# Kernel tuning notes

Hardware: AMD Instinct MI355X
Metric: run time of the kernel (lower is better)

Reference implementation:

```python
import jax, jax.numpy as jnp
import numpy as np

SCALE = 1.0

def setup_inputs() -> dict:
    key = jax.random.key(0)
    k1, k2 = jax.random.split(key)
    template = jax.random.normal(k1, (4, 8192, 3), dtype=jnp.float32)
    source = jax.random.normal(k2, (4, 8192, 3), dtype=jnp.float32)
    return {"template": template, "source": source}

def _chamfer(p0, p1):
    # p0: [B,N,3], p1: [B,M,3]
    # squared pairwise distances: [B,N,M]
    sq0 = jnp.sum(p0 * p0, axis=-1)  # [B,N]
    sq1 = jnp.sum(p1 * p1, axis=-1)  # [B,M]
    cross = jnp.einsum('bnd,bmd->bnm', p0, p1)
    d = sq0[:, :, None] + sq1[:, None, :] - 2.0 * cross  # [B,N,M]
    d = jnp.maximum(d, 0.0)
    cost_p0_p1 = jnp.min(d, axis=2)  # [B,N] min sq dist p0 -> p1
    cost_p1_p0 = jnp.min(d, axis=1)  # [B,M] min sq dist p1 -> p0
    c01 = jnp.mean(jnp.sqrt(cost_p0_p1), axis=-1)  # [B]
    c10 = jnp.mean(jnp.sqrt(cost_p1_p0), axis=-1)  # [B]
    return (c01 + c10) / 2.0  # [B]

def reference(template, source):
    p0 = template / SCALE
    p1 = source / SCALE
    per_batch = _chamfer(p0, p1)
    return jnp.mean(per_batch, axis=0)  # reduction='mean' -> scalar
```

## Files before the change

kernel.cpp:

```cpp
#include <hip/hip_runtime.h>
#include <math.h>

#define NPTS 8192
#define NB 4
#define BLK 256
#define Q 8
#define TILE 512

__global__ __launch_bounds__(BLK) void chamfer_partial(
    const float* __restrict__ tmpl, const float* __restrict__ src,
    float* __restrict__ partial, int seg_len, int nseg)
{
    __shared__ float4 lds[TILE];
    const int bd  = blockIdx.z;
    const int b   = bd >> 1;
    const int dir = bd & 1;
    const float* qp = (dir ? src : tmpl) + (size_t)b * NPTS * 3;
    const float* rp = (dir ? tmpl : src) + (size_t)b * NPTS * 3;
    const int tid   = threadIdx.x;
    const int qbase = blockIdx.x * (BLK * Q);

    float qx[Q], qy[Q], qz[Q], mn[Q];
#pragma unroll
    for (int k = 0; k < Q; k++) {
        const int qi = qbase + k * BLK + tid;
        qx[k] = qp[3 * qi + 0];
        qy[k] = qp[3 * qi + 1];
        qz[k] = qp[3 * qi + 2];
        mn[k] = 3.4e38f;
    }

    const int seg_start = blockIdx.y * seg_len;
    for (int ts = 0; ts < seg_len; ts += TILE) {
        __syncthreads();
        for (int i = tid; i < TILE; i += BLK) {
            const int ri = seg_start + ts + i;
            const float rx = rp[3 * ri + 0];
            const float ry = rp[3 * ri + 1];
            const float rz = rp[3 * ri + 2];
            lds[i] = make_float4(-2.f * rx, -2.f * ry, -2.f * rz,
                                 rx * rx + ry * ry + rz * rz);
        }
        __syncthreads();
#pragma unroll 4
        for (int j = 0; j < TILE; j++) {
            const float4 r = lds[j];
#pragma unroll
            for (int k = 0; k < Q; k++) {
                float t = fmaf(qx[k], r.x, r.w);
                t = fmaf(qy[k], r.y, t);
                t = fmaf(qz[k], r.z, t);
                mn[k] = fminf(mn[k], t);
            }
        }
    }

    const size_t base = ((size_t)bd * nseg + blockIdx.y) * NPTS;
#pragma unroll
    for (int k = 0; k < Q; k++)
        partial[base + qbase + k * BLK + tid] = mn[k];
}

__global__ __launch_bounds__(BLK) void chamfer_reduce(
    const float* __restrict__ tmpl, const float* __restrict__ src,
    const float* __restrict__ partial, float* __restrict__ out, int nseg)
{
    const int t  = blockIdx.x * BLK + threadIdx.x;
    const int bd = t >> 13;
    const int qi = t & (NPTS - 1);
    const int b  = bd >> 1;
    const int dir = bd & 1;
    const float* qp = (dir ? src : tmpl) + (size_t)b * NPTS * 3;
    const float qx = qp[3 * qi + 0];
    const float qy = qp[3 * qi + 1];
    const float qz = qp[3 * qi + 2];
    const float sq = qx * qx + qy * qy + qz * qz;

    float m = 3.4e38f;
    for (int s = 0; s < nseg; s++)
        m = fminf(m, partial[((size_t)bd * nseg + s) * NPTS + qi]);

    float v = sqrtf(fmaxf(sq + m, 0.f));

#pragma unroll
    for (int off = 32; off > 0; off >>= 1)
        v += __shfl_down(v, off, 64);

    __shared__ float wsum[BLK / 64];
    const int lane = threadIdx.x & 63;
    const int wid  = threadIdx.x >> 6;
    if (lane == 0) wsum[wid] = v;
    __syncthreads();
    if (threadIdx.x == 0) {
        float s = 0.f;
#pragma unroll
        for (int w = 0; w < BLK / 64; w++) s += wsum[w];
        atomicAdd(out, s * (1.0f / 65536.0f));
    }
}

extern "C" void kernel_launch(void* const* d_in, const int* in_sizes, int n_in,
                              void* d_out, int out_size, void* d_ws, size_t ws_size,
                              hipStream_t stream) {
    const float* tmpl = (const float*)d_in[0];
    const float* src  = (const float*)d_in[1];
    float* out      = (float*)d_out;
    float* partial  = (float*)d_ws;

    int nseg = 16;
    while (nseg > 1 && (size_t)8 * nseg * NPTS * sizeof(float) > ws_size)
        nseg >>= 1;
    const int seg_len = NPTS / nseg;

    hipMemsetAsync(d_out, 0, sizeof(float), stream);

    dim3 g1(NPTS / (BLK * Q), nseg, 2 * NB);
    chamfer_partial<<<g1, BLK, 0, stream>>>(tmpl, src, partial, seg_len, nseg);

    chamfer_reduce<<<(2 * NB * NPTS) / BLK, BLK, 0, stream>>>(tmpl, src, partial, out, nseg);
}
```

Measured before the change: 104.7 us.

## Compute pairwise distances with bf16 split-precision MFMA and min3 reductions

Replaces the scalar FMA distance loop with 32x32x16 bf16 MFMA. A pack kernel splits each coordinate, its -2x scale and its squared norm into hi/lo bf16 pairs, so one MFMA yields a near-fp32 squared-distance term. Reference tiles are double-buffered through LDS, and the per-query minimum is taken with v_min3. This moves the O(N^2) arithmetic onto matrix cores at the cost of an extra pack kernel and somewhat reduced precision, since the lo*lo cross terms are dropped.

New measurement: 93.03 us. 1.13x faster.

```diff
diff --git a/kernel.cpp b/kernel.cpp
--- a/kernel.cpp
+++ b/kernel.cpp
@@ -4,66 +4,121 @@
 #define NPTS 8192
 #define NB 4
 #define BLK 256
-#define Q 8
-#define TILE 512
 
-__global__ __launch_bounds__(BLK) void chamfer_partial(
+typedef __attribute__((ext_vector_type(8))) short  short8v;
+typedef __attribute__((ext_vector_type(16))) float f32x16;
+
+__device__ __forceinline__ float min3f(float a, float b, float c) {
+    float d;
+    asm("v_min3_f32 %0, %1, %2, %3" : "=v"(d) : "v"(a), "v"(b), "v"(c));
+    return d;
+}
+__device__ __forceinline__ unsigned short f2bf(float f) {
+    unsigned u = __float_as_uint(f);
+    return (unsigned short)((u + 0x7FFFu + ((u >> 16) & 1u)) >> 16);
+}
+__device__ __forceinline__ float bf2f(unsigned short h) {
+    return __uint_as_float(((unsigned)h) << 16);
+}
+
+__global__ __launch_bounds__(BLK) void chamfer_pack(
     const float* __restrict__ tmpl, const float* __restrict__ src,
-    float* __restrict__ partial, int seg_len, int nseg)
+    short* __restrict__ apack, short* __restrict__ bpack)
 {
-    __shared__ float4 lds[TILE];
+    const int t   = blockIdx.x * BLK + threadIdx.x;
+    const int arr = t >> 15;
+    const int b   = (t >> 13) & 3;
+    const int i   = t & (NPTS - 1);
+    const float* p = (arr ? src : tmpl) + ((size_t)b * NPTS + i) * 3;
+    const float x = p[0], y = p[1], z = p[2];
+
+    const unsigned short xh = f2bf(x), yh = f2bf(y), zh = f2bf(z);
+    const unsigned short xl = f2bf(x - bf2f(xh));
+    const unsigned short yl = f2bf(y - bf2f(yh));
+    const unsigned short zl = f2bf(z - bf2f(zh));
+    const float w = fmaf(x, x, fmaf(y, y, z * z));
+    const unsigned short wh = f2bf(w);
+    const unsigned short wl = f2bf(w - bf2f(wh));
+    const float mx = -2.f * x, my = -2.f * y, mz = -2.f * z;
+    const unsigned short mxh = f2bf(mx), myh = f2bf(my), mzh = f2bf(mz);
+    const unsigned short mxl = f2bf(mx - bf2f(mxh));
+    const unsigned short myl = f2bf(my - bf2f(myh));
+    const unsigned short mzl = f2bf(mz - bf2f(mzh));
+    const unsigned short ONE = 0x3F80;
+
+    const size_t base = (size_t)(arr * 4 + b) * (NPTS * 16);
+    const int    tl   = i >> 5, lr = i & 31;
+    short* ap = apack + base + (size_t)tl * 512;
+    short* bp = bpack + base + (size_t)tl * 512;
+
+    const short8v a0 = {(short)xh, (short)yh, (short)zh, (short)xl,
+                        (short)yl, (short)zl, (short)xh, (short)yh};
+    const short8v a1 = {(short)zh, (short)wh, (short)wl, 0, 0, 0, 0, 0};
+    *(short8v*)(ap + lr * 8)        = a0;
+    *(short8v*)(ap + (lr + 32) * 8) = a1;
+
+    const short8v b0 = {(short)mxh, (short)myh, (short)mzh, (short)mxh,
+                        (short)myh, (short)mzh, (short)mxl, (short)myl};
+    const short8v b1 = {(short)mzl, (short)ONE, (short)ONE, 0, 0, 0, 0, 0};
+    *(short8v*)(bp + lr * 8)        = b0;
+    *(short8v*)(bp + (lr + 32) * 8) = b1;
+}
+
+__global__ __launch_bounds__(BLK) void chamfer_mfma(
+    const short* __restrict__ apack, const short* __restrict__ bpack,
+    float* __restrict__ partial)
+{
+    __shared__ __align__(16) short lds[2][8192];
     const int bd  = blockIdx.z;
-    const int b   = bd >> 1;
-    const int dir = bd & 1;
-    const float* qp = (dir ? src : tmpl) + (size_t)b * NPTS * 3;
-    const float* rp = (dir ? tmpl : src) + (size_t)b * NPTS * 3;
-    const int tid   = threadIdx.x;
-    const int qbase = blockIdx.x * (BLK * Q);
+    const int seg = blockIdx.y;
+    const int qb  = blockIdx.x;
+    const int b = bd >> 1, dir = bd & 1;
+    const short* ab = apack + (size_t)((dir ^ 1) * 4 + b) * (NPTS * 16)
+                            + (size_t)seg * 128 * 512;
+    const short* bb = bpack + (size_t)(dir * 4 + b) * (NPTS * 16);
+    const int tid = threadIdx.x, wid = tid >> 6, lane = tid & 63;
 
-    float qx[Q], qy[Q], qz[Q], mn[Q];
+    const int qt = qb * 4 + wid;
+    const short8v bfrag = *(const short8v*)(bb + (size_t)qt * 512 + lane * 8);
+
+    float mn = 3.4e38f;
+    short8v st[4];
+#define LOADREGS(c) { const short* s_ = ab + (size_t)(c) * 8192;               \
+    _Pragma("unroll") for (int i_ = 0; i_ < 4; i_++)                           \
+        st[i_] = *(const short8v*)(s_ + i_ * 2048 + tid * 8); }
+#define WRITEBUF(bf) { _Pragma("unroll") for (int i_ = 0; i_ < 4; i_++)        \
+        *(short8v*)(&lds[bf][i_ * 2048 + tid * 8]) = st[i_]; }
+
+    LOADREGS(0); WRITEBUF(0); LOADREGS(1);
+    __syncthreads();
+    for (int c = 0; c < 8; c++) {
+        if (c + 1 < 8) WRITEBUF((c + 1) & 1);
+        if (c + 2 < 8) LOADREGS(c + 2);
+        const short* lbase = &lds[c & 1][lane * 8];
 #pragma unroll
-    for (int k = 0; k < Q; k++) {
-        const int qi = qbase + k * BLK + tid;
-        qx[k] = qp[3 * qi + 0];
-        qy[k] = qp[3 * qi + 1];
-        qz[k] = qp[3 * qi + 2];
-        mn[k] = 3.4e38f;
-    }
-
-    const int seg_start = blockIdx.y * seg_len;
-    for (int ts = 0; ts < seg_len; ts += TILE) {
-        __syncthreads();
-        for (int i = tid; i < TILE; i += BLK) {
-            const int ri = seg_start + ts + i;
-            const float rx = rp[3 * ri + 0];
-            const float ry = rp[3 * ri + 1];
-            const float rz = rp[3 * ri + 2];
-            lds[i] = make_float4(-2.f * rx, -2.f * ry, -2.f * rz,
-                                 rx * rx + ry * ry + rz * rz);
+        for (int t = 0; t < 16; t++) {
+            const short8v a = *(const short8v*)(lbase + t * 512);
+            f32x16 d = __builtin_amdgcn_mfma_f32_32x32x16_bf16(
+                a, bfrag, (f32x16)(0.f), 0, 0, 0);
+            const float g0 = min3f(d[0],  d[1],  d[2]);
+            const float g1 = min3f(d[3],  d[4],  d[5]);
+            const float g2 = min3f(d[6],  d[7],  d[8]);
+            const float g3 = min3f(d[9],  d[10], d[11]);
+            const float g4 = min3f(d[12], d[13], d[14]);
+            mn = min3f(mn, g0, g1);
+            mn = min3f(mn, g2, g3);
+            mn = min3f(mn, g4, d[15]);
         }
         __syncthreads();
-#pragma unroll 4
-        for (int j = 0; j < TILE; j++) {
-            const float4 r = lds[j];
-#pragma unroll
-            for (int k = 0; k < Q; k++) {
-                float t = fmaf(qx[k], r.x, r.w);
-                t = fmaf(qy[k], r.y, t);
-                t = fmaf(qz[k], r.z, t);
-                mn[k] = fminf(mn[k], t);
-            }
-        }
     }
-
-    const size_t base = ((size_t)bd * nseg + blockIdx.y) * NPTS;
-#pragma unroll
-    for (int k = 0; k < Q; k++)
-        partial[base + qbase + k * BLK + tid] = mn[k];
+    mn = fminf(mn, __shfl_xor(mn, 32, 64));
+    if (lane < 32)
+        partial[((size_t)bd * 2 + seg) * NPTS + qt * 32 + lane] = mn;
 }
 
 __global__ __launch_bounds__(BLK) void chamfer_reduce(
     const float* __restrict__ tmpl, const float* __restrict__ src,
-    const float* __restrict__ partial, float* __restrict__ out, int nseg)
+    const float* __restrict__ partial, float* __restrict__ out)
 {
     const int t  = blockIdx.x * BLK + threadIdx.x;
     const int bd = t >> 13;
@@ -76,10 +131,8 @@
     const float qz = qp[3 * qi + 2];
     const float sq = qx * qx + qy * qy + qz * qz;
 
-    float m = 3.4e38f;
-    for (int s = 0; s < nseg; s++)
-        m = fminf(m, partial[((size_t)bd * nseg + s) * NPTS + qi]);
-
+    const float m = fminf(partial[((size_t)bd * 2 + 0) * NPTS + qi],
+                          partial[((size_t)bd * 2 + 1) * NPTS + qi]);
     float v = sqrtf(fmaxf(sq + m, 0.f));
 
 #pragma unroll
@@ -104,18 +157,18 @@
                               hipStream_t stream) {
     const float* tmpl = (const float*)d_in[0];
     const float* src  = (const float*)d_in[1];
-    float* out      = (float*)d_out;
-    float* partial  = (float*)d_ws;
+    float* out = (float*)d_out;
 
-    int nseg = 16;
-    while (nseg > 1 && (size_t)8 * nseg * NPTS * sizeof(float) > ws_size)
-        nseg >>= 1;
-    const int seg_len = NPTS / nseg;
+    short* apack   = (short*)d_ws;
+    short* bpack   = apack + (size_t)8 * NPTS * 16;
+    float* partial = (float*)(bpack + (size_t)8 * NPTS * 16);
 
     hipMemsetAsync(d_out, 0, sizeof(float), stream);
 
-    dim3 g1(NPTS / (BLK * Q), nseg, 2 * NB);
-    chamfer_partial<<<g1, BLK, 0, stream>>>(tmpl, src, partial, seg_len, nseg);
+    chamfer_pack<<<(2 * NB * NPTS) / BLK, BLK, 0, stream>>>(tmpl, src, apack, bpack);
 
-    chamfer_reduce<<<(2 * NB * NPTS) / BLK, BLK, 0, stream>>>(tmpl, src, partial, out, nseg);
+    dim3 g1(NPTS / 128, 2, 2 * NB);
+    chamfer_mfma<<<g1, BLK, 0, stream>>>(apack, bpack, partial);
+
+    chamfer_reduce<<<(2 * NB * NPTS) / BLK, BLK, 0, stream>>>(tmpl, src, partial, out);
 }
```
